# Kernel tuning notes

Hardware: AMD Instinct MI355X
Metric: run time of the kernel (lower is better)

Reference implementation:

```python
import jax, jax.numpy as jnp
import numpy as np

N = 50000
E = 200000
H = 8          # heads
C = 256        # out channels per head
IN = 256       # in_dim
NEG_SLOPE = 0.2
EPS = 1e-16    # PyG softmax denominator epsilon


def setup_inputs() -> dict:
    key = jax.random.key(0)
    k1, k2, k3, k4, k5, k6 = jax.random.split(key, 6)
    glorot = lambda k, shape, fan: jax.random.normal(k, shape, jnp.float32) * np.sqrt(2.0 / fan)
    x = jax.random.normal(k1, (N, IN), jnp.float32)
    edge_index = jax.random.randint(k2, (2, E), 0, N, jnp.int32)
    W = glorot(k3, (IN, H * C), IN + H * C)          # lin_src weight (shared src/dst)
    att_src = glorot(k4, (H, C), C)
    att_dst = glorot(k5, (H, C), C)
    bias = jnp.zeros((C,), jnp.float32)              # concat=False -> bias size out_dim
    return {"x": x, "edge_index": edge_index, "W": W,
            "att_src": att_src, "att_dst": att_dst, "bias": bias}


def reference(x, edge_index, W, att_src, att_dst, bias):
    # Linear projection -> per-head features [N, H, C]
    h = (x @ W).reshape(N, H, C)
    # Per-node attention logits [N, H]
    a_src = jnp.einsum('nhc,hc->nh', h, att_src)
    a_dst = jnp.einsum('nhc,hc->nh', h, att_dst)
    src, dst = edge_index[0], edge_index[1]
    # Edge scores with leaky relu [E, H]
    e = jax.nn.leaky_relu(a_src[src] + a_dst[dst], NEG_SLOPE)
    # Segment softmax over incoming edges of each dst node
    m = jax.ops.segment_max(e, dst, num_segments=N)          # [N, H]
    e = jnp.exp(e - m[dst])
    denom = jax.ops.segment_sum(e, dst, num_segments=N)      # [N, H]
    alpha = e / (denom[dst] + EPS)                           # [E, H]
    # Weighted scatter-add aggregation [N, H, C]
    msg = h[src] * alpha[:, :, None]
    out = jax.ops.segment_sum(msg, dst, num_segments=N)
    # concat=False -> mean over heads, then bias
    return out.mean(axis=1) + bias
```

## Files before the change

kernel.cpp:

```cpp
#include <hip/hip_runtime.h>
#include <hip/hip_bf16.h>

#define NN 50000
#define EE 200000
#define HH 8
#define CC 256
#define IND 256
#define HC 2048
#define NEG 0.2f
#define EPSV 1e-16f

typedef __attribute__((ext_vector_type(8))) short short8;
typedef __attribute__((ext_vector_type(4))) float f32x4;

__device__ __forceinline__ float b2f(unsigned short u) {
  return __uint_as_float(((unsigned)u) << 16);
}
__device__ __forceinline__ unsigned short f2b(float f) {
  unsigned u = __float_as_uint(f);
  unsigned r = (u + 0x7FFFu + ((u >> 16) & 1u)) >> 16;
  return (unsigned short)r;
}

__global__ __launch_bounds__(1024) void k_wt2(const float* __restrict__ W,
                                              unsigned short* __restrict__ wt2) {
  __shared__ float tile[32][33];
  int kk0 = blockIdx.x * 32;
  int c0 = blockIdx.y * 32;
  int tx = threadIdx.x & 31, ty = threadIdx.x >> 5;
  int h = kk0 >> 8;
  int k = (kk0 & 255) + ty;
  tile[ty][tx] = W[(size_t)k * HC + h * 256 + c0 + tx] * 0.125f;
  __syncthreads();
  wt2[(size_t)(c0 + ty) * HC + kk0 + tx] = f2b(tile[tx][ty]);
}

__global__ __launch_bounds__(256) void k_wfold(const float* __restrict__ W,
                                               const float* __restrict__ att_s,
                                               const float* __restrict__ att_d,
                                               float* __restrict__ wsrc,
                                               float* __restrict__ wdst) {
  int in = blockIdx.x;
  int t = threadIdx.x;
  int h = t >> 5;
  int c0 = (t & 31) * 8;
  float ps = 0.f, pd = 0.f;
#pragma unroll
  for (int j = 0; j < 8; ++j) {
    float wv = W[(size_t)in * HC + h * 256 + c0 + j];
    ps += wv * att_s[h * 256 + c0 + j];
    pd += wv * att_d[h * 256 + c0 + j];
  }
#pragma unroll
  for (int o = 16; o >= 1; o >>= 1) {
    ps += __shfl_down(ps, o, 32);
    pd += __shfl_down(pd, o, 32);
  }
  if ((t & 31) == 0) {
    wsrc[in * HH + h] = ps;
    wdst[in * HH + h] = pd;
  }
}

__global__ __launch_bounds__(256) void k_alog2c(const float* __restrict__ x,
                                                const float* __restrict__ wsrc,
                                                const float* __restrict__ wdst,
                                                unsigned short* __restrict__ xb,
                                                float* __restrict__ a_src,
                                                float* __restrict__ a_dst) {
  const int l = threadIdx.x & 63;
  const int gwave = (blockIdx.x * 256 + threadIdx.x) >> 6;
  const int nwaves = (gridDim.x * 256) >> 6;
  float ws_[4][8], wd_[4][8];
#pragma unroll
  for (int j = 0; j < 4; ++j) {
#pragma unroll
    for (int h = 0; h < 8; ++h) {
      ws_[j][h] = wsrc[(l * 4 + j) * HH + h];
      wd_[j][h] = wdst[(l * 4 + j) * HH + h];
    }
  }
  for (int n = gwave; n < NN; n += nwaves) {
    float4 xv = *(const float4*)(x + (size_t)n * IND + l * 4);
    float xa[4] = {xv.x, xv.y, xv.z, xv.w};
    ushort4 o = make_ushort4(f2b(xv.x), f2b(xv.y), f2b(xv.z), f2b(xv.w));
    *(ushort4*)(xb + (size_t)n * IND + l * 4) = o;
    float as[8] = {}, ad[8] = {};
#pragma unroll
    for (int j = 0; j < 4; ++j)
#pragma unroll
      for (int h = 0; h < 8; ++h) {
        as[h] += xa[j] * ws_[j][h];
        ad[h] += xa[j] * wd_[j][h];
      }
#pragma unroll
    for (int o2 = 32; o2 >= 1; o2 >>= 1) {
#pragma unroll
      for (int h = 0; h < 8; ++h) {
        as[h] += __shfl_down(as[h], o2);
        ad[h] += __shfl_down(ad[h], o2);
      }
    }
    if (l == 0) {
#pragma unroll
      for (int h = 0; h < 8; ++h) {
        a_src[n * HH + h] = as[h];
        a_dst[n * HH + h] = ad[h];
      }
    }
  }
}

__global__ void k_hist(const int* __restrict__ dstn, int* __restrict__ deg) {
  int e = blockIdx.x * 256 + threadIdx.x;
  if (e < EE) atomicAdd(&deg[dstn[e]], 1);
}

__global__ __launch_bounds__(1024) void k_scanA(const int* __restrict__ deg,
                                                int* __restrict__ incl, int* __restrict__ bsum) {
  __shared__ int s[1024];
  int tid = threadIdx.x;
  int i = blockIdx.x * 1024 + tid;
  s[tid] = (i < NN) ? deg[i] : 0;
  __syncthreads();
  for (int o = 1; o < 1024; o <<= 1) {
    int add = (tid >= o) ? s[tid - o] : 0;
    __syncthreads();
    s[tid] += add;
    __syncthreads();
  }
  if (i < NN) incl[i] = s[tid];
  if (tid == 1023) bsum[blockIdx.x] = s[1023];
}

__global__ void k_scanB(int* bsum, int nb) {
  if (threadIdx.x == 0 && blockIdx.x == 0) {
    int run = 0;
    for (int b = 0; b < nb; ++b) { int v = bsum[b]; bsum[b] = run; run += v; }
  }
}

__global__ __launch_bounds__(1024) void k_scanC(const int* __restrict__ deg, const int* __restrict__ incl,
                                                const int* __restrict__ bsum, int* __restrict__ row_start,
                                                int* __restrict__ cursor) {
  int i = blockIdx.x * 1024 + threadIdx.x;
  if (i < NN) {
    int ex = bsum[i >> 10] + incl[i] - deg[i];
    row_start[i] = ex;
    cursor[i] = ex;
  }
  if (i == 0) row_start[NN] = EE;
}

__global__ void k_scatter(const int* __restrict__ srcn, const int* __restrict__ dstn,
                          int* __restrict__ cursor, int* __restrict__ csr_src) {
  int e = blockIdx.x * 256 + threadIdx.x;
  if (e < EE) {
    int d = dstn[e];
    int p = atomicAdd(&cursor[d], 1);
    csr_src[p] = srcn[e];
  }
}

__global__ __launch_bounds__(256) void k_aggxf(const unsigned short* __restrict__ xb,
                                               const float* __restrict__ a_src,
                                               const float* __restrict__ a_dst,
                                               const int* __restrict__ row_start,
                                               const int* __restrict__ csr_src,
                                               unsigned short* __restrict__ y) {
  __shared__ float alpha_s[4][8][8];
  const int l = threadIdx.x & 63;
  const int wv = threadIdx.x >> 6;
  const int n = blockIdx.x * 4 + wv;
  if (n >= NN) return;
  const int start = row_start[n];
  const int D = row_start[n + 1] - start;
  unsigned short* yp = y + (size_t)n * HC + l * 4;
  if (D == 0) {
    ushort4 z = make_ushort4(0, 0, 0, 0);
#pragma unroll
    for (int h = 0; h < 8; ++h) *(ushort4*)(yp + h * 256) = z;
    return;
  }
  const int h = l & 7;
  const int e8 = l >> 3;
  const float adst = a_dst[n * HH + h];

  int s0 = 0;
  float lg0 = -INFINITY;
  if (e8 < D) {
    s0 = csr_src[start + e8];
    float xv = a_src[s0 * HH + h] + adst;
    lg0 = (xv > 0.f) ? xv : NEG * xv;
  }
  float m = lg0;
  float ss = (e8 < D) ? 1.f : 0.f;
  for (int base = 8; base < D; base += 8) {
    int e = base + e8;
    float lg = -INFINITY;
    if (e < D) {
      int s = csr_src[start + e];
      float xv = a_src[s * HH + h] + adst;
      lg = (xv > 0.f) ? xv : NEG * xv;
    }
    if (lg > m) { ss *= __expf(m - lg); m = lg; }
    if (e < D) ss += __expf(lg - m);
  }
#pragma unroll
  for (int mask = 8; mask < 64; mask <<= 1) {
    float mo = __shfl_xor(m, mask, 64);
    float so = __shfl_xor(ss, mask, 64);
    float nm = fmaxf(m, mo);
    float s1 = (m == -INFINITY) ? 0.f : ss * __expf(m - nm);
    float s2 = (mo == -INFINITY) ? 0.f : so * __expf(mo - nm);
    m = nm;
    ss = s1 + s2;
  }
  const float inv = 1.f / (ss + EPSV);

  float acc[8][4] = {};
  for (int base = 0; base < D; base += 8) {
    int nch = min(8, D - base);
    int s;
    float lg;
    if (base == 0) {
      s = s0;
      lg = lg0;
    } else {
      int e = base + e8;
      s = 0;
      lg = -INFINITY;
      if (e < D) {
        s = csr_src[start + e];
        float xv = a_src[s * HH + h] + adst;
        lg = (xv > 0.f) ? xv : NEG * xv;
      }
    }
    float al = __expf(lg - m) * inv;
    alpha_s[wv][e8][h] = al;
    for (int e = 0; e < nch; ++e) {
      int se = __shfl(s, e * 8, 64);
      f32x4 a0 = *(const f32x4*)&alpha_s[wv][e][0];
      f32x4 a1 = *(const f32x4*)&alpha_s[wv][e][4];
      ushort4 v = *(const ushort4*)(xb + (size_t)se * IND + l * 4);
      float x0 = b2f(v.x), x1 = b2f(v.y), x2 = b2f(v.z), x3 = b2f(v.w);
#pragma unroll
      for (int hh = 0; hh < 8; ++hh) {
        float a = (hh < 4) ? a0[hh] : a1[hh - 4];
        acc[hh][0] += a * x0;
        acc[hh][1] += a * x1;
        acc[hh][2] += a * x2;
        acc[hh][3] += a * x3;
      }
    }
  }
#pragma unroll
  for (int hh = 0; hh < 8; ++hh) {
    ushort4 o = make_ushort4(f2b(acc[hh][0]), f2b(acc[hh][1]), f2b(acc[hh][2]), f2b(acc[hh][3]));
    *(ushort4*)(yp + hh * 256) = o;
  }
}

__global__ __launch_bounds__(512) void k_gemm2(const unsigned short* __restrict__ y,
                                               const unsigned short* __restrict__ wt2,
                                               const float* __restrict__ bias,
                                               float* __restrict__ out) {
  __shared__ unsigned short As[128 * 64];
  __shared__ unsigned short Bs[256 * 64];
  const int t = threadIdx.x;
  const int lane = t & 63;
  const int w = t >> 6;
  const int wr = w >> 2;
  const int wc = w & 3;
  const int l16 = lane & 15;
  const int lq = lane >> 4;
  const int m0 = blockIdx.x * 128;

  f32x4 acc[4][4] = {};

  const int so = t * 16;

  for (int ks = 0; ks < 32; ++ks) {
    const int k0 = ks * 64;
#pragma unroll
    for (int i = 0; i < 2; ++i) {
      int o = i * 8192 + so;
      int row = o >> 7;
      int cg = ((o >> 4) & 7) ^ (row & 7);
      const unsigned short* srcA = y + (size_t)(m0 + row) * HC + k0 + cg * 8;
      __builtin_amdgcn_global_load_lds(
          (const __attribute__((address_space(1))) void*)srcA,
          (__attribute__((address_space(3))) void*)((char*)As + o), 16, 0, 0);
    }
#pragma unroll
    for (int i = 0; i < 4; ++i) {
      int o = i * 8192 + so;
      int row = o >> 7;
      int cg = ((o >> 4) & 7) ^ (row & 7);
      const unsigned short* srcB = wt2 + (size_t)row * HC + k0 + cg * 8;
      __builtin_amdgcn_global_load_lds(
          (const __attribute__((address_space(1))) void*)srcB,
          (__attribute__((address_space(3))) void*)((char*)Bs + o), 16, 0, 0);
    }
    __syncthreads();
#pragma unroll
    for (int kk = 0; kk < 2; ++kk) {
      short8 af[4], bf[4];
#pragma unroll
      for (int m = 0; m < 4; ++m) {
        int row = wr * 64 + m * 16 + l16;
        int byte = row * 128 + (((kk * 4 + lq) ^ (row & 7)) << 4);
        af[m] = *(const short8*)((const char*)As + byte);
      }
#pragma unroll
      for (int n = 0; n < 4; ++n) {
        int row = wc * 64 + n * 16 + l16;
        int byte = row * 128 + (((kk * 4 + lq) ^ (row & 7)) << 4);
        bf[n] = *(const short8*)((const char*)Bs + byte);
      }
      __builtin_amdgcn_s_setprio(1);
#pragma unroll
      for (int m = 0; m < 4; ++m)
#pragma unroll
        for (int n = 0; n < 4; ++n)
          acc[m][n] = __builtin_amdgcn_mfma_f32_16x16x32_bf16(af[m], bf[n], acc[m][n], 0, 0, 0);
      __builtin_amdgcn_s_setprio(0);
    }
    __syncthreads();
  }

  const int r0 = lq * 4;
#pragma unroll
  for (int n = 0; n < 4; ++n) {
    int gcol = wc * 64 + n * 16 + l16;
    float bv = bias[gcol];
#pragma unroll
    for (int m = 0; m < 4; ++m) {
#pragma unroll
      for (int r = 0; r < 4; ++r) {
        int grow = m0 + wr * 64 + m * 16 + r0 + r;
        if (grow < NN) out[(size_t)grow * CC + gcol] = acc[m][n][r] + bv;
      }
    }
  }
}

extern "C" void kernel_launch(void* const* d_in, const int* in_sizes, int n_in,
                              void* d_out, int out_size, void* d_ws, size_t ws_size,
                              hipStream_t stream) {
  (void)in_sizes; (void)n_in; (void)out_size; (void)ws_size;
  const float* x = (const float*)d_in[0];
  const int* ei = (const int*)d_in[1];
  const float* W = (const float*)d_in[2];
  const float* att_s = (const float*)d_in[3];
  const float* att_d = (const float*)d_in[4];
  const float* bias = (const float*)d_in[5];
  float* out = (float*)d_out;
  const int* srcp = ei;
  const int* dstp = ei + EE;

  char* ws = (char*)d_ws;
  size_t off = 0;
  auto alloc = [&](size_t bytes) {
    void* p = ws + off;
    off = (off + bytes + 255) & ~(size_t)255;
    return p;
  };
  unsigned short* y = (unsigned short*)alloc((size_t)NN * HC * 2);
  unsigned short* xb = (unsigned short*)alloc((size_t)NN * IND * 2);
  unsigned short* wt2 = (unsigned short*)alloc((size_t)HC * IND * 2);
  float* wsrc = (float*)alloc((size_t)IND * HH * 4);
  float* wdst = (float*)alloc((size_t)IND * HH * 4);
  float* a_src = (float*)alloc((size_t)NN * HH * 4);
  float* a_dst = (float*)alloc((size_t)NN * HH * 4);
  int* deg = (int*)alloc((size_t)NN * 4);
  int* incl = (int*)alloc((size_t)NN * 4);
  int* row_start = (int*)alloc((size_t)(NN + 1) * 4);
  int* cursor = (int*)alloc((size_t)NN * 4);
  int* csr_src = (int*)alloc((size_t)EE * 4);
  int* bsum = (int*)alloc(256);

  hipMemsetAsync(deg, 0, (size_t)NN * 4, stream);

  k_wt2<<<dim3(HC / 32, CC / 32), 1024, 0, stream>>>(W, wt2);
  k_wfold<<<IND, 256, 0, stream>>>(W, att_s, att_d, wsrc, wdst);
  k_alog2c<<<832, 256, 0, stream>>>(x, wsrc, wdst, xb, a_src, a_dst);
  k_hist<<<(EE + 255) / 256, 256, 0, stream>>>(dstp, deg);
  int nb = (NN + 1023) / 1024;
  k_scanA<<<nb, 1024, 0, stream>>>(deg, incl, bsum);
  k_scanB<<<1, 64, 0, stream>>>(bsum, nb);
  k_scanC<<<nb, 1024, 0, stream>>>(deg, incl, bsum, row_start, cursor);
  k_scatter<<<(EE + 255) / 256, 256, 0, stream>>>(srcp, dstp, cursor, csr_src);
  k_aggxf<<<(NN + 3) / 4, 256, 0, stream>>>(xb, a_src, a_dst, row_start, csr_src, y);
  k_gemm2<<<(NN + 127) / 128, 512, 0, stream>>>(y, wt2, bias, out);
}
```

Baseline: 251.2 us.

## Single-pass unnormalized softmax aggregation, fuse degree histogram, warp-parallel block scan

The aggregation kernel no longer runs a separate pass to find the per-head max and sum. It accumulates exp(clamped logit)-weighted features and the running sum in one pass, then scales by the reciprocal sum at the end. This removes one round of CSR and a_src gathers and the extra exp work. The degree histogram is folded into the logit kernel, saving a launch, and the block-sum scan uses a wave shuffle scan instead of a serial single thread. The catch is that skipping max subtraction relies on logits staying below the clamp of 60. Larger logits would be silently distorted.

```diff
diff --git a/kernel.cpp b/kernel.cpp
--- a/kernel.cpp
+++ b/kernel.cpp
@@ -65,9 +65,14 @@
 __global__ __launch_bounds__(256) void k_alog2c(const float* __restrict__ x,
                                                 const float* __restrict__ wsrc,
                                                 const float* __restrict__ wdst,
+                                                const int* __restrict__ dstn,
                                                 unsigned short* __restrict__ xb,
                                                 float* __restrict__ a_src,
-                                                float* __restrict__ a_dst) {
+                                                float* __restrict__ a_dst,
+                                                int* __restrict__ deg) {
+  int gid = blockIdx.x * 256 + threadIdx.x;
+  if (gid < EE) atomicAdd(&deg[dstn[gid]], 1);
+
   const int l = threadIdx.x & 63;
   const int gwave = (blockIdx.x * 256 + threadIdx.x) >> 6;
   const int nwaves = (gridDim.x * 256) >> 6;
@@ -109,11 +114,6 @@
       }
     }
   }
-}
-
-__global__ void k_hist(const int* __restrict__ dstn, int* __restrict__ deg) {
-  int e = blockIdx.x * 256 + threadIdx.x;
-  if (e < EE) atomicAdd(&deg[dstn[e]], 1);
 }
 
 __global__ __launch_bounds__(1024) void k_scanA(const int* __restrict__ deg,
@@ -134,10 +134,15 @@
 }
 
 __global__ void k_scanB(int* bsum, int nb) {
-  if (threadIdx.x == 0 && blockIdx.x == 0) {
-    int run = 0;
-    for (int b = 0; b < nb; ++b) { int v = bsum[b]; bsum[b] = run; run += v; }
-  }
+  int l = threadIdx.x & 63;
+  int v = (l < nb) ? bsum[l] : 0;
+  int incl = v;
+#pragma unroll
+  for (int o = 1; o < 64; o <<= 1) {
+    int t = __shfl_up(incl, o, 64);
+    if (l >= o) incl += t;
+  }
+  if (l < nb) bsum[l] = incl - v;
 }
 
 __global__ __launch_bounds__(1024) void k_scanC(const int* __restrict__ deg, const int* __restrict__ incl,
@@ -168,7 +173,8 @@
                                                const int* __restrict__ row_start,
                                                const int* __restrict__ csr_src,
                                                unsigned short* __restrict__ y) {
-  __shared__ float alpha_s[4][8][8];
+  __shared__ float w_s[4][8][8];
+  __shared__ float inv_s[4][8];
   const int l = threadIdx.x & 63;
   const int wv = threadIdx.x >> 6;
   const int n = blockIdx.x * 4 + wv;
@@ -186,62 +192,25 @@
   const int e8 = l >> 3;
   const float adst = a_dst[n * HH + h];
 
-  int s0 = 0;
-  float lg0 = -INFINITY;
-  if (e8 < D) {
-    s0 = csr_src[start + e8];
-    float xv = a_src[s0 * HH + h] + adst;
-    lg0 = (xv > 0.f) ? xv : NEG * xv;
-  }
-  float m = lg0;
-  float ss = (e8 < D) ? 1.f : 0.f;
-  for (int base = 8; base < D; base += 8) {
-    int e = base + e8;
-    float lg = -INFINITY;
-    if (e < D) {
-      int s = csr_src[start + e];
-      float xv = a_src[s * HH + h] + adst;
-      lg = (xv > 0.f) ? xv : NEG * xv;
-    }
-    if (lg > m) { ss *= __expf(m - lg); m = lg; }
-    if (e < D) ss += __expf(lg - m);
-  }
-#pragma unroll
-  for (int mask = 8; mask < 64; mask <<= 1) {
-    float mo = __shfl_xor(m, mask, 64);
-    float so = __shfl_xor(ss, mask, 64);
-    float nm = fmaxf(m, mo);
-    float s1 = (m == -INFINITY) ? 0.f : ss * __expf(m - nm);
-    float s2 = (mo == -INFINITY) ? 0.f : so * __expf(mo - nm);
-    m = nm;
-    ss = s1 + s2;
-  }
-  const float inv = 1.f / (ss + EPSV);
-
+  float ssum = 0.f;
   float acc[8][4] = {};
   for (int base = 0; base < D; base += 8) {
     int nch = min(8, D - base);
-    int s;
-    float lg;
-    if (base == 0) {
-      s = s0;
-      lg = lg0;
-    } else {
-      int e = base + e8;
-      s = 0;
-      lg = -INFINITY;
-      if (e < D) {
-        s = csr_src[start + e];
-        float xv = a_src[s * HH + h] + adst;
-        lg = (xv > 0.f) ? xv : NEG * xv;
-      }
-    }
-    float al = __expf(lg - m) * inv;
-    alpha_s[wv][e8][h] = al;
-    for (int e = 0; e < nch; ++e) {
-      int se = __shfl(s, e * 8, 64);
-      f32x4 a0 = *(const f32x4*)&alpha_s[wv][e][0];
-      f32x4 a1 = *(const f32x4*)&alpha_s[wv][e][4];
+    int e = base + e8;
+    int s = 0;
+    float we = 0.f;
+    if (e < D) {
+      s = csr_src[start + e];
+      float xv = a_src[s * HH + h] + adst;
+      float lg = (xv > 0.f) ? xv : NEG * xv;
+      we = __expf(fminf(lg, 60.f));
+      ssum += we;
+    }
+    w_s[wv][e8][h] = we;
+    for (int ee = 0; ee < nch; ++ee) {
+      int se = __shfl(s, ee * 8, 64);
+      f32x4 a0 = *(const f32x4*)&w_s[wv][ee][0];
+      f32x4 a1 = *(const f32x4*)&w_s[wv][ee][4];
       ushort4 v = *(const ushort4*)(xb + (size_t)se * IND + l * 4);
       float x0 = b2f(v.x), x1 = b2f(v.y), x2 = b2f(v.z), x3 = b2f(v.w);
 #pragma unroll
@@ -255,8 +224,15 @@
     }
   }
 #pragma unroll
+  for (int mask = 8; mask < 64; mask <<= 1) ssum += __shfl_xor(ssum, mask, 64);
+  if (e8 == 0) inv_s[wv][h] = 1.f / (ssum + EPSV);
+  f32x4 i0 = *(const f32x4*)&inv_s[wv][0];
+  f32x4 i1 = *(const f32x4*)&inv_s[wv][4];
+#pragma unroll
   for (int hh = 0; hh < 8; ++hh) {
-    ushort4 o = make_ushort4(f2b(acc[hh][0]), f2b(acc[hh][1]), f2b(acc[hh][2]), f2b(acc[hh][3]));
+    float iv = (hh < 4) ? i0[hh] : i1[hh - 4];
+    ushort4 o = make_ushort4(f2b(acc[hh][0] * iv), f2b(acc[hh][1] * iv),
+                             f2b(acc[hh][2] * iv), f2b(acc[hh][3] * iv));
     *(ushort4*)(yp + hh * 256) = o;
   }
 }
@@ -384,8 +360,7 @@
 
   k_wt2<<<dim3(HC / 32, CC / 32), 1024, 0, stream>>>(W, wt2);
   k_wfold<<<IND, 256, 0, stream>>>(W, att_s, att_d, wsrc, wdst);
-  k_alog2c<<<832, 256, 0, stream>>>(x, wsrc, wdst, xb, a_src, a_dst);
-  k_hist<<<(EE + 255) / 256, 256, 0, stream>>>(dstp, deg);
+  k_alog2c<<<832, 256, 0, stream>>>(x, wsrc, wdst, dstp, xb, a_src, a_dst, deg);
   int nb = (NN + 1023) / 1024;
   k_scanA<<<nb, 1024, 0, stream>>>(deg, incl, bsum);
   k_scanB<<<1, 64, 0, stream>>>(bsum, nb);
```

New measurement: 242.7 us. 1.04x faster.
